# Kernel tuning notes

Measured on AMD Instinct MI355X. Metric: run time of the kernel, lower is better.

The kernel has to match this reference:

```python
import jax, jax.numpy as jnp
import numpy as np

HIDDEN = 2048
NHEADS = 16
NKV = 4
HEAD_DIM = 128
B, T = 2, 2048


def setup_inputs() -> dict:
    key = jax.random.key(0)
    ks = jax.random.split(key, 7)
    x = jax.random.normal(ks[0], (B, T, HIDDEN), dtype=jnp.float32)
    # rope tables [T, head_dim//2]
    inv_freq = 1.0 / (10000.0 ** (jnp.arange(0, HEAD_DIM // 2, dtype=jnp.float32) / (HEAD_DIM // 2)))
    pos = jnp.arange(T, dtype=jnp.float32)
    ang = pos[:, None] * inv_freq[None, :]
    cos, sin = jnp.cos(ang), jnp.sin(ang)
    s = 0.02
    wq = jax.random.normal(ks[1], (HIDDEN, NHEADS * HEAD_DIM), dtype=jnp.float32) * s
    wk = jax.random.normal(ks[2], (HIDDEN, NKV * HEAD_DIM), dtype=jnp.float32) * s
    wv = jax.random.normal(ks[3], (HIDDEN, NKV * HEAD_DIM), dtype=jnp.float32) * s
    wo = jax.random.normal(ks[4], (NHEADS * HEAD_DIM, HIDDEN), dtype=jnp.float32) * s
    return {"x": x, "cos": cos, "sin": sin, "wq": wq, "wk": wk, "wv": wv, "wo": wo}


def _apply_rope(x, cos, sin):
    # x: [B, H, T, D]; cos/sin: [T, D//2]
    hd = x.shape[-1]
    x1, x2 = x[..., : hd // 2], x[..., hd // 2 :]
    c = cos[None, None, : x.shape[2], :]
    s = sin[None, None, : x.shape[2], :]
    return jnp.concatenate([x1 * c - x2 * s, x2 * c + x1 * s], axis=-1)


def reference(x, cos, sin, wq, wk, wv, wo):
    Bb, Tt, _ = x.shape
    q = (x @ wq).reshape(Bb, Tt, NHEADS, HEAD_DIM).transpose(0, 2, 1, 3)  # [B,H,T,D]
    k = (x @ wk).reshape(Bb, Tt, NKV, HEAD_DIM).transpose(0, 2, 1, 3)    # [B,Hk,T,D]
    v = (x @ wv).reshape(Bb, Tt, NKV, HEAD_DIM).transpose(0, 2, 1, 3)
    q = _apply_rope(q, cos, sin)
    k = _apply_rope(k, cos, sin)
    groups = NHEADS // NKV
    k = jnp.repeat(k, groups, axis=1)  # [B,H,T,D]
    v = jnp.repeat(v, groups, axis=1)
    scale = 1.0 / jnp.sqrt(jnp.asarray(HEAD_DIM, dtype=x.dtype))
    scores = jnp.einsum("bhqd,bhkd->bhqk", q, k) * scale
    causal = jnp.tril(jnp.ones((Tt, Tt), dtype=bool))
    scores = jnp.where(causal[None, None, :, :], scores, jnp.asarray(-jnp.inf, dtype=scores.dtype))
    attn = jax.nn.softmax(scores, axis=-1)
    out = jnp.einsum("bhqk,bhkd->bhqd", attn, v)
    out = out.transpose(0, 2, 1, 3).reshape(Bb, Tt, NHEADS * HEAD_DIM)
    return out @ wo
```

## Files before the change

kernel.cpp:

```cpp
#include <hip/hip_runtime.h>

#define HIDDEN 2048
#define NHEADS 16
#define NKV 4
#define HEAD_DIM 128
#define BB 2
#define TT 2048
#define MROWS (BB * TT)
#define NQKV (NHEADS * HEAD_DIM + 2 * NKV * HEAD_DIM)

typedef __attribute__((ext_vector_type(8))) short short8;
typedef __attribute__((ext_vector_type(4))) float f32x4;

#if __has_builtin(__builtin_amdgcn_exp2f)
#define EXP2F __builtin_amdgcn_exp2f
#else
#define EXP2F exp2f
#endif

__device__ __forceinline__ unsigned short f2bf(float f) {
    unsigned int u = __float_as_uint(f);
    unsigned int r = u + 0x7fffu + ((u >> 16) & 1u);
    return (unsigned short)(r >> 16);
}
__device__ __forceinline__ float b2f(unsigned short h) {
    return __uint_as_float(((unsigned int)h) << 16);
}

__device__ __forceinline__ void store_out(float* p, float v) { *p = v; }
__device__ __forceinline__ void store_out(unsigned short* p, float v) { *p = f2bf(v); }

__device__ __forceinline__ void load_lds_16(const void* g, void* l) {
    __builtin_amdgcn_global_load_lds((const __attribute__((address_space(1))) unsigned int*)g,
                                     (__attribute__((address_space(3))) unsigned int*)l,
                                     16, 0, 0);
}

__global__ void cast_x_kernel(const float* __restrict__ x, unsigned short* __restrict__ xb) {
    int i = blockIdx.x * 256 + threadIdx.x;
    float4 v = ((const float4*)x)[i];
    ushort4 o;
    o.x = f2bf(v.x); o.y = f2bf(v.y); o.z = f2bf(v.z); o.w = f2bf(v.w);
    ((ushort4*)xb)[i] = o;
}

__global__ void pack_wqkvT_kernel(const float* __restrict__ wq, const float* __restrict__ wk,
                                  const float* __restrict__ wv, unsigned short* __restrict__ out) {
    __shared__ float tile[32][33];
    int n0 = blockIdx.x * 32, k0 = blockIdx.y * 32;
    int tx = threadIdx.x, ty = threadIdx.y;
#pragma unroll
    for (int i = 0; i < 32; i += 8) {
        int k = k0 + ty + i;
        int n = n0 + tx;
        float v;
        if (n < 2048)      v = wq[(size_t)k * 2048 + n];
        else if (n < 2560) v = wk[(size_t)k * 512 + (n - 2048)];
        else               v = wv[(size_t)k * 512 + (n - 2560)];
        tile[ty + i][tx] = v;
    }
    __syncthreads();
#pragma unroll
    for (int i = 0; i < 32; i += 8) {
        int n = n0 + ty + i;
        int k = k0 + tx;
        out[(size_t)n * HIDDEN + k] = f2bf(tile[tx][ty + i]);
    }
}

__global__ void pack_woT_kernel(const float* __restrict__ wo, unsigned short* __restrict__ out) {
    __shared__ float tile[32][33];
    int n0 = blockIdx.x * 32, k0 = blockIdx.y * 32;
    int tx = threadIdx.x, ty = threadIdx.y;
#pragma unroll
    for (int i = 0; i < 32; i += 8)
        tile[ty + i][tx] = wo[(size_t)(k0 + ty + i) * HIDDEN + n0 + tx];
    __syncthreads();
#pragma unroll
    for (int i = 0; i < 32; i += 8)
        out[(size_t)(n0 + ty + i) * HIDDEN + k0 + tx] = f2bf(tile[tx][ty + i]);
}

template <typename OutT>
__global__ __launch_bounds__(512, 2) void gemm256_kernel(const unsigned short* __restrict__ A,
                                                         const unsigned short* __restrict__ Bt,
                                                         OutT* __restrict__ C,
                                                         int M, int N, int K, int NBX) {
    __shared__ __align__(16) unsigned short sbuf[2][2][256 * 64];
    const int tid = threadIdx.x;
    const int lane = tid & 63, w = tid >> 6;
    const int quad = lane >> 4, l15 = lane & 15;
    const int wrM = w >> 2, wcN = w & 3;

    const int nwg = gridDim.x;
    const int bswz = (blockIdx.x & 7) * (nwg >> 3) + (blockIdx.x >> 3);
    const int m0 = (bswz / NBX) * 256;
    const int n0 = (bswz % NBX) * 256;

    const int lr = tid >> 3;
    const int sc = (tid & 7) ^ (lr & 7);
    const unsigned short* gA = A + (size_t)(m0 + lr) * K + sc * 8;
    const unsigned short* gB = Bt + (size_t)(n0 + lr) * K + sc * 8;
    const size_t jstep = (size_t)64 * K;

    const int s0 = (quad ^ (l15 & 7)) * 8;
    const int s1 = ((4 | quad) ^ (l15 & 7)) * 8;

    f32x4 acc[8][4];
    const f32x4 z4 = {0.f, 0.f, 0.f, 0.f};
#pragma unroll
    for (int mi = 0; mi < 8; ++mi)
#pragma unroll
        for (int ni = 0; ni < 4; ++ni) acc[mi][ni] = z4;

#pragma unroll
    for (int j = 0; j < 4; ++j) {
        load_lds_16(gA + (size_t)j * jstep, &sbuf[0][0][j * 4096 + w * 512]);
        load_lds_16(gB + (size_t)j * jstep, &sbuf[0][1][j * 4096 + w * 512]);
    }
    __asm__ volatile("s_waitcnt vmcnt(0)" ::: "memory");
    __builtin_amdgcn_s_barrier();

    const int NT = K >> 6;
    for (int kt = 0; kt < NT; ++kt) {
        const int buf = kt & 1;
        const unsigned short* bA = &sbuf[buf][0][0];
        const unsigned short* bB = &sbuf[buf][1][0];

        if (kt + 1 < NT) {
            const size_t kof = (size_t)(kt + 1) * 64;
#pragma unroll
            for (int j = 0; j < 4; ++j) {
                load_lds_16(gA + (size_t)j * jstep + kof, &sbuf[buf ^ 1][0][j * 4096 + w * 512]);
                load_lds_16(gB + (size_t)j * jstep + kof, &sbuf[buf ^ 1][1][j * 4096 + w * 512]);
            }
        }

        short8 bf0[4], bf1[4];
#pragma unroll
        for (int ni = 0; ni < 4; ++ni) {
            const unsigned short* br = bB + (wcN * 64 + ni * 16 + l15) * 64;
            bf0[ni] = *(const short8*)(br + s0);
            bf1[ni] = *(const short8*)(br + s1);
        }

#pragma unroll
        for (int ph = 0; ph < 4; ++ph) {
            short8 af0[2], af1[2];
#pragma unroll
            for (int mm = 0; mm < 2; ++mm) {
                const unsigned short* ar = bA + (wrM * 128 + (ph * 2 + mm) * 16 + l15) * 64;
                af0[mm] = *(const short8*)(ar + s0);
                af1[mm] = *(const short8*)(ar + s1);
            }
            if (ph == 3 && kt + 1 < NT) {
                __asm__ volatile("s_waitcnt vmcnt(0)" ::: "memory");
            }
            __builtin_amdgcn_s_barrier();
            __asm__ volatile("s_waitcnt lgkmcnt(0)" ::: "memory");
            __builtin_amdgcn_s_setprio(1);
#pragma unroll
            for (int mm = 0; mm < 2; ++mm)
#pragma unroll
                for (int ni = 0; ni < 4; ++ni) {
                    acc[ph * 2 + mm][ni] =
                        __builtin_amdgcn_mfma_f32_16x16x32_bf16(af0[mm], bf0[ni], acc[ph * 2 + mm][ni], 0, 0, 0);
                    acc[ph * 2 + mm][ni] =
                        __builtin_amdgcn_mfma_f32_16x16x32_bf16(af1[mm], bf1[ni], acc[ph * 2 + mm][ni], 0, 0, 0);
                }
            __builtin_amdgcn_s_setprio(0);
            __builtin_amdgcn_s_barrier();
        }
    }

#pragma unroll
    for (int mi = 0; mi < 8; ++mi)
#pragma unroll
        for (int ni = 0; ni < 4; ++ni)
#pragma unroll
            for (int r = 0; r < 4; ++r) {
                int gr = m0 + wrM * 128 + mi * 16 + quad * 4 + r;
                int gc = n0 + wcN * 64 + ni * 16 + l15;
                store_out(&C[(size_t)gr * N + gc], acc[mi][ni][r]);
            }
}

__global__ __launch_bounds__(512, 2) void gemm256n128_kernel(const unsigned short* __restrict__ A,
                                                             const unsigned short* __restrict__ Bt,
                                                             float* __restrict__ C,
                                                             int M, int N, int K, int NBX) {
    __shared__ __align__(16) unsigned short sA[2][256 * 64];
    __shared__ __align__(16) unsigned short sB[2][128 * 64];
    const int tid = threadIdx.x;
    const int lane = tid & 63, w = tid >> 6;
    const int quad = lane >> 4, l15 = lane & 15;
    const int wrM = w >> 1, wcN = w & 1;

    const int nwg = gridDim.x;
    const int bswz = (blockIdx.x & 7) * (nwg >> 3) + (blockIdx.x >> 3);
    const int m0 = (bswz / NBX) * 256;
    const int n0 = (bswz % NBX) * 128;

    const int lr = tid >> 3;
    const int sc = (tid & 7) ^ (lr & 7);
    const unsigned short* gA = A + (size_t)(m0 + lr) * K + sc * 8;
    const unsigned short* gB = Bt + (size_t)(n0 + lr) * K + sc * 8;
    const size_t jstep = (size_t)64 * K;

    const int s0 = (quad ^ (l15 & 7)) * 8;
    const int s1 = ((4 | quad) ^ (l15 & 7)) * 8;

    f32x4 acc[4][4];
    const f32x4 z4 = {0.f, 0.f, 0.f, 0.f};
#pragma unroll
    for (int mi = 0; mi < 4; ++mi)
#pragma unroll
        for (int ni = 0; ni < 4; ++ni) acc[mi][ni] = z4;

#pragma unroll
    for (int j = 0; j < 4; ++j)
        load_lds_16(gA + (size_t)j * jstep, &sA[0][j * 4096 + w * 512]);
#pragma unroll
    for (int j = 0; j < 2; ++j)
        load_lds_16(gB + (size_t)j * jstep, &sB[0][j * 4096 + w * 512]);
    __asm__ volatile("s_waitcnt vmcnt(0)" ::: "memory");
    __builtin_amdgcn_s_barrier();

    const int NT = K >> 6;
    for (int kt = 0; kt < NT; ++kt) {
        const int buf = kt & 1;
        const unsigned short* bA = &sA[buf][0];
        const unsigned short* bB = &sB[buf][0];

        if (kt + 1 < NT) {
            const size_t kof = (size_t)(kt + 1) * 64;
#pragma unroll
            for (int j = 0; j < 4; ++j)
                load_lds_16(gA + (size_t)j * jstep + kof, &sA[buf ^ 1][j * 4096 + w * 512]);
#pragma unroll
            for (int j = 0; j < 2; ++j)
                load_lds_16(gB + (size_t)j * jstep + kof, &sB[buf ^ 1][j * 4096 + w * 512]);
        }

        short8 bf0[4], bf1[4];
#pragma unroll
        for (int ni = 0; ni < 4; ++ni) {
            const unsigned short* br = bB + (wcN * 64 + ni * 16 + l15) * 64;
            bf0[ni] = *(const short8*)(br + s0);
            bf1[ni] = *(const short8*)(br + s1);
        }

#pragma unroll
        for (int ph = 0; ph < 4; ++ph) {
            short8 af0, af1;
            {
                const unsigned short* ar = bA + (wrM * 64 + ph * 16 + l15) * 64;
                af0 = *(const short8*)(ar + s0);
                af1 = *(const short8*)(ar + s1);
            }
            if (ph == 3 && kt + 1 < NT) {
                __asm__ volatile("s_waitcnt vmcnt(0)" ::: "memory");
            }
            __builtin_amdgcn_s_barrier();
            __asm__ volatile("s_waitcnt lgkmcnt(0)" ::: "memory");
            __builtin_amdgcn_s_setprio(1);
#pragma unroll
            for (int ni = 0; ni < 4; ++ni) {
                acc[ph][ni] = __builtin_amdgcn_mfma_f32_16x16x32_bf16(af0, bf0[ni], acc[ph][ni], 0, 0, 0);
                acc[ph][ni] = __builtin_amdgcn_mfma_f32_16x16x32_bf16(af1, bf1[ni], acc[ph][ni], 0, 0, 0);
            }
            __builtin_amdgcn_s_setprio(0);
            __builtin_amdgcn_s_barrier();
        }
    }

#pragma unroll
    for (int mi = 0; mi < 4; ++mi)
#pragma unroll
        for (int ni = 0; ni < 4; ++ni)
#pragma unroll
            for (int r = 0; r < 4; ++r) {
                int gr = m0 + wrM * 64 + mi * 16 + quad * 4 + r;
                int gc = n0 + wcN * 64 + ni * 16 + l15;
                C[(size_t)gr * N + gc] = acc[mi][ni][r];
            }
}

#define QP (MROWS * NHEADS * 64)
#define KP (MROWS * NKV * 64)
#define QSCL (0.08838834764831845f * 1.4426950408889634f)
__global__ void rope_kernel(const unsigned short* __restrict__ qkv,
                            const float* __restrict__ cosb, const float* __restrict__ sinb,
                            unsigned short* __restrict__ Q, unsigned short* __restrict__ K) {
    int tid = blockIdx.x * 256 + threadIdx.x;
    if (tid < QP) {
        int d = tid & 63;
        int h = (tid >> 6) & 15;
        int row = tid >> 10;
        int t = row & (TT - 1), b = row >> 11;
        float x1 = b2f(qkv[(size_t)row * NQKV + h * 128 + d]);
        float x2 = b2f(qkv[(size_t)row * NQKV + h * 128 + d + 64]);
        float c = cosb[t * 64 + d], s = sinb[t * 64 + d];
        unsigned short* dst = Q + ((size_t)(b * NHEADS + h) * TT + t) * 128 + d;
        dst[0]  = f2bf((x1 * c - x2 * s) * QSCL);
        dst[64] = f2bf((x2 * c + x1 * s) * QSCL);
    } else {
        int p = tid - QP;
        int d = p & 63;
        int kh = (p >> 6) & 3;
        int row = p >> 8;
        int t = row & (TT - 1), b = row >> 11;
        float x1 = b2f(qkv[(size_t)row * NQKV + 2048 + kh * 128 + d]);
        float x2 = b2f(qkv[(size_t)row * NQKV + 2048 + kh * 128 + d + 64]);
        float c = cosb[t * 64 + d], s = sinb[t * 64 + d];
        unsigned short* dst = K + ((size_t)(b * NKV + kh) * TT + t) * 128 + d;
        dst[0]  = f2bf(x1 * c - x2 * s);
        dst[64] = f2bf(x2 * c + x1 * s);
    }
}

__global__ void vtrans_kernel(const unsigned short* __restrict__ qkv,
                              unsigned short* __restrict__ Vt) {
    __shared__ unsigned short tile[32][33];
    int t0 = blockIdx.x * 32, d0 = blockIdx.y * 32, bz = blockIdx.z;
    int b = bz >> 2, kh = bz & 3;
    int tx = threadIdx.x, ty = threadIdx.y;
#pragma unroll
    for (int i = 0; i < 32; i += 8)
        tile[ty + i][tx] = qkv[(size_t)(b * TT + t0 + ty + i) * NQKV + 2560 + kh * 128 + d0 + tx];
    __syncthreads();
#pragma unroll
    for (int i = 0; i < 32; i += 8)
        Vt[((size_t)bz * 128 + d0 + ty + i) * TT + t0 + tx] = tile[tx][ty + i];
}

__global__ __launch_bounds__(256, 3) void flash_kernel(const unsigned short* __restrict__ Qb,
                                                       const unsigned short* __restrict__ Kb,
                                                       const unsigned short* __restrict__ Vtb,
                                                       unsigned short* __restrict__ Ob,
                                                       unsigned short* __restrict__ Po,
                                                       float* __restrict__ Pl) {
    __shared__ __align__(16) unsigned short sK[2][64 * 128];
    __shared__ __align__(16) unsigned short sV[128 * 64];

    const int tid = threadIdx.x;
    const int w = tid >> 6, lane = tid & 63;
    const int quad = lane >> 4, l15 = lane & 15;
    const int r7 = l15 & 7;

    const int lin = blockIdx.x;
    const int member = lin >> 8;
    const int rem = lin & 255;
    const int h = rem & 15;
    const int b = (rem >> 4) & 1;
    const int j = rem >> 5;
    int qb, kvlo, kvhi;
    bool partial;
    if (member == 2) {
        qb = j; kvlo = 0; kvhi = (qb + 1) * 128; partial = false;
    } else {
        qb = 15 - j;
        int half = (qb + 1) * 64;
        kvlo = member ? half : 0;
        kvhi = member ? (qb + 1) * 128 : half;
        partial = true;
    }
    const int q0 = qb * 128;
    const int ntile = (kvhi - kvlo) >> 6;
    const int kvh = h >> 2;
    const unsigned short* Qh = Qb + (size_t)(b * NHEADS + h) * TT * 128;
    const unsigned short* Kh = Kb + (size_t)(b * NKV + kvh) * TT * 128;
    const unsigned short* Vth = Vtb + (size_t)(b * NKV + kvh) * 128 * TT;

    const int wrow0 = q0 + w * 32;

    const int kr = lane >> 4;
    const unsigned short* gKe = Kh + (size_t)(w * 16 + kr) * 128 + (((lane & 15) ^ kr) * 8);
    const unsigned short* gKo = Kh + (size_t)(w * 16 + 4 + kr) * 128 + (((lane & 15) ^ (4 + kr)) * 8);
    const int vr = lane >> 3;
    const unsigned short* gV0 = Vth + (size_t)(w * 32 + vr) * TT + (((lane & 7) ^ vr) * 8);

    short8 aq[2][4];
#pragma unroll
    for (int mi = 0; mi < 2; ++mi)
#pragma unroll
        for (int dk = 0; dk < 4; ++dk)
            aq[mi][dk] = *(const short8*)(Qh + (size_t)(wrow0 + mi * 16 + l15) * 128 + dk * 32 + quad * 8);

    f32x4 accO[2][8];
    float accLc[2] = {0.f, 0.f};
    const f32x4 z4 = {0.f, 0.f, 0.f, 0.f};
#pragma unroll
    for (int mi = 0; mi < 2; ++mi)
#pragma unroll
        for (int nb = 0; nb < 8; ++nb) accO[mi][nb] = z4;

#pragma unroll
    for (int g = 0; g < 4; ++g) {
        const unsigned short* src = (g & 1) ? gKo : gKe;
        load_lds_16(src + (size_t)(kvlo + (g >> 1) * 8) * 128, &sK[0][(w * 4 + g) * 512]);
    }

    for (int it = 0; it < ntile; ++it) {
        const int cur = it & 1;
        const int kv0 = kvlo + it * 64;
        __asm__ volatile("s_waitcnt vmcnt(0)" ::: "memory");
        __builtin_amdgcn_s_barrier();
#pragma unroll
        for (int g = 0; g < 4; ++g)
            load_lds_16(gV0 + (size_t)(g * 8) * TT + kv0, &sV[(w * 4 + g) * 512]);
        const bool hasn = (it + 1 < ntile);
        if (hasn) {
#pragma unroll
            for (int g = 0; g < 4; ++g) {
                const unsigned short* src = (g & 1) ? gKo : gKe;
                load_lds_16(src + (size_t)(kv0 + 64 + (g >> 1) * 8) * 128, &sK[cur ^ 1][(w * 4 + g) * 512]);
            }
        }
        const bool compute = (kv0 <= wrow0 + 31);
        short8 ap[2][2];
        if (compute) {
            f32x4 st[4][2];
#pragma unroll
            for (int t = 0; t < 4; ++t)
#pragma unroll
                for (int h2 = 0; h2 < 2; ++h2) st[t][h2] = z4;
            __builtin_amdgcn_s_setprio(1);
#pragma unroll
            for (int t = 0; t < 4; ++t) {
#pragma unroll
                for (int dk = 0; dk < 4; ++dk) {
                    short8 ak = *(const short8*)(&sK[cur][(t * 16 + l15) * 128 + ((dk * 4 + quad) ^ r7) * 8]);
                    st[t][0] = __builtin_amdgcn_mfma_f32_16x16x32_bf16(ak, aq[0][dk], st[t][0], 0, 0, 0);
                    st[t][1] = __builtin_amdgcn_mfma_f32_16x16x32_bf16(ak, aq[1][dk], st[t][1], 0, 0, 0);
                }
            }
            __builtin_amdgcn_s_setprio(0);
            unsigned int pk32[4][2][2];
#pragma unroll
            for (int h2 = 0; h2 < 2; ++h2) {
                const int qg = wrow0 + h2 * 16 + l15;
#pragma unroll
                for (int t = 0; t < 4; ++t) {
                    const int kvb = kv0 + t * 16 + quad * 4;
                    const bool nm = (kv0 + t * 16 + 15) > (wrow0 + h2 * 16);
                    float pv[4];
#pragma unroll
                    for (int r = 0; r < 4; ++r) {
                        float p = EXP2F(st[t][h2][r]);
                        if (nm) p = (kvb + r <= qg) ? p : 0.f;
                        pv[r] = p;
                    }
                    accLc[h2] += (pv[0] + pv[1]) + (pv[2] + pv[3]);
                    __asm__("v_cvt_pk_bf16_f32 %0, %1, %2" : "=v"(pk32[t][h2][0]) : "v"(pv[0]), "v"(pv[1]));
                    __asm__("v_cvt_pk_bf16_f32 %0, %1, %2" : "=v"(pk32[t][h2][1]) : "v"(pv[2]), "v"(pv[3]));
                }
            }
#pragma unroll
            for (int h2 = 0; h2 < 2; ++h2)
#pragma unroll
                for (int kf = 0; kf < 2; ++kf) {
                    union { unsigned int u[4]; short8 s8; } W;
#pragma unroll
                    for (int wdx = 0; wdx < 4; ++wdx) {
                        int srcl = (2 * (quad & 1) + (wdx >> 1)) * 16 + l15;
                        unsigned int a0 = (unsigned int)__shfl((int)pk32[2 * kf][h2][wdx & 1], srcl, 64);
                        unsigned int a1 = (unsigned int)__shfl((int)pk32[2 * kf + 1][h2][wdx & 1], srcl, 64);
                        W.u[wdx] = (quad >> 1) ? a1 : a0;
                    }
                    ap[h2][kf] = W.s8;
                }
        }
        if (hasn) { __asm__ volatile("s_waitcnt vmcnt(4)" ::: "memory"); }
        else      { __asm__ volatile("s_waitcnt vmcnt(0)" ::: "memory"); }
        __builtin_amdgcn_s_barrier();
        if (compute) {
            __builtin_amdgcn_s_setprio(1);
#pragma unroll
            for (int nb = 0; nb < 8; ++nb) {
                short8 bv0 = *(const short8*)(&sV[(nb * 16 + l15) * 64 + ((quad) ^ r7) * 8]);
                short8 bv1 = *(const short8*)(&sV[(nb * 16 + l15) * 64 + ((4 + quad) ^ r7) * 8]);
#pragma unroll
                for (int mi = 0; mi < 2; ++mi) {
                    accO[mi][nb] = __builtin_amdgcn_mfma_f32_16x16x32_bf16(ap[mi][0], bv0, accO[mi][nb], 0, 0, 0);
                    accO[mi][nb] = __builtin_amdgcn_mfma_f32_16x16x32_bf16(ap[mi][1], bv1, accO[mi][nb], 0, 0, 0);
                }
            }
            __builtin_amdgcn_s_setprio(0);
        }
    }

    float Lr[2][4];
#pragma unroll
    for (int mi = 0; mi < 2; ++mi) {
        float v = accLc[mi];
        v += __shfl_xor(v, 16, 64);
        v += __shfl_xor(v, 32, 64);
#pragma unroll
        for (int r = 0; r < 4; ++r)
            Lr[mi][r] = __shfl(v, quad * 4 + r, 64);
    }

    __syncthreads();
    unsigned short* sPw = &sV[w * 2048];

    if (!partial) {
        float inv[2][4];
#pragma unroll
        for (int mi = 0; mi < 2; ++mi)
#pragma unroll
            for (int r = 0; r < 4; ++r) inv[mi][r] = 1.0f / Lr[mi][r];
        const size_t obase = ((size_t)b * TT + wrow0) * (NHEADS * HEAD_DIM) + h * 128;
#pragma unroll
        for (int half = 0; half < 2; ++half) {
            __asm__ volatile("s_waitcnt lgkmcnt(0)" ::: "memory");
#pragma unroll
            for (int mi = 0; mi < 2; ++mi)
#pragma unroll
                for (int nb2 = 0; nb2 < 4; ++nb2)
#pragma unroll
                    for (int r = 0; r < 4; ++r) {
                        const int row = mi * 16 + quad * 4 + r;
                        sPw[row * 64 + (((2 * nb2 + (l15 >> 3)) ^ (row & 7)) * 8) + r7] =
                            f2bf(accO[mi][half * 4 + nb2][r] * inv[mi][r]);
                    }
            __asm__ volatile("s_waitcnt lgkmcnt(0)" ::: "memory");
#pragma unroll
            for (int pass = 0; pass < 4; ++pass) {
                int row2 = pass * 8 + (lane >> 3);
                short8 vv = *(const short8*)(&sPw[row2 * 64 + (((lane & 7) ^ (row2 & 7)) * 8)]);
                *(short8*)(Ob + obase + (size_t)row2 * (NHEADS * HEAD_DIM) + half * 64 + (lane & 7) * 8) = vv;
            }
        }
    } else {
        const size_t pbase = ((size_t)(member * 2 + b) * 1024 + (wrow0 - 1024)) * 2048 + h * 128;
#pragma unroll
        for (int half = 0; half < 2; ++half) {
            __asm__ volatile("s_waitcnt lgkmcnt(0)" ::: "memory");
#pragma unroll
            for (int mi = 0; mi < 2; ++mi)
#pragma unroll
                for (int nb2 = 0; nb2 < 4; ++nb2)
#pragma unroll
                    for (int r = 0; r < 4; ++r) {
                        const int row = mi * 16 + quad * 4 + r;
                        sPw[row * 64 + (((2 * nb2 + (l15 >> 3)) ^ (row & 7)) * 8) + r7] =
                            f2bf(accO[mi][half * 4 + nb2][r]);
                    }
            __asm__ volatile("s_waitcnt lgkmcnt(0)" ::: "memory");
#pragma unroll
            for (int pass = 0; pass < 4; ++pass) {
                int row2 = pass * 8 + (lane >> 3);
                short8 vv = *(const short8*)(&sPw[row2 * 64 + (((lane & 7) ^ (row2 & 7)) * 8)]);
                *(short8*)(Po + pbase + (size_t)row2 * 2048 + half * 64 + (lane & 7) * 8) = vv;
            }
        }
        float* plb = Pl + ((size_t)(member * 2 + b) * 16 + h) * 1024 + (wrow0 - 1024);
        if (l15 == 0) {
#pragma unroll
            for (int mi = 0; mi < 2; ++mi)
#pragma unroll
                for (int r = 0; r < 4; ++r)
                    plb[mi * 16 + quad * 4 + r] = Lr[mi][r];
        }
    }
}

__global__ void merge_kernel(const unsigned short* __restrict__ Po, const float* __restrict__ Pl,
                             unsigned short* __restrict__ attn) {
    int gid = blockIdx.x * 256 + threadIdx.x;
    size_t e8 = (size_t)gid * 8;
    int col = (int)(e8 & 2047);
    int rl  = (int)((e8 >> 11) & 1023);
    int b   = (int)(e8 >> 21);
    int h   = col >> 7;
    size_t i0 = ((size_t)b * 1024 + rl) * 2048 + col;
    size_t i1 = ((size_t)(2 + b) * 1024 + rl) * 2048 + col;
    float l = Pl[((size_t)b * 16 + h) * 1024 + rl] + Pl[((size_t)(2 + b) * 16 + h) * 1024 + rl];
    float inv = 1.0f / l;
    union { uint4 v; unsigned short u[8]; } a, c, o;
    a.v = *(const uint4*)(Po + i0);
    c.v = *(const uint4*)(Po + i1);
#pragma unroll
    for (int k = 0; k < 8; ++k)
        o.u[k] = f2bf((b2f(a.u[k]) + b2f(c.u[k])) * inv);
    *(uint4*)(attn + ((size_t)b * 2048 + 1024 + rl) * 2048 + col) = o.v;
}

extern "C" void kernel_launch(void* const* d_in, const int* in_sizes, int n_in,
                              void* d_out, int out_size, void* d_ws, size_t ws_size,
                              hipStream_t stream) {
    const float* x    = (const float*)d_in[0];
    const float* cosb = (const float*)d_in[1];
    const float* sinb = (const float*)d_in[2];
    const float* wq   = (const float*)d_in[3];
    const float* wk   = (const float*)d_in[4];
    const float* wv   = (const float*)d_in[5];
    const float* wo   = (const float*)d_in[6];
    float* out = (float*)d_out;

    char* ws = (char*)d_ws;
    unsigned short* xb    = (unsigned short*)(ws);
    unsigned short* wqkvT = (unsigned short*)(ws + (16u << 20));
    unsigned short* woT   = (unsigned short*)(ws + (28u << 20));
    unsigned short* qkv   = (unsigned short*)(ws + (36u << 20));
    unsigned short* Qbuf  = (unsigned short*)(ws + (60u << 20));
    unsigned short* Kbuf  = (unsigned short*)(ws + (76u << 20));
    unsigned short* Vt    = (unsigned short*)(ws + (80u << 20));
    unsigned short* attn  = (unsigned short*)(ws + (84u << 20));
    unsigned short* Po    = (unsigned short*)(ws);
    float*          Pl    = (float*)(ws + (16u << 20));

    cast_x_kernel<<<(MROWS * HIDDEN) / 4 / 256, 256, 0, stream>>>(x, xb);
    pack_wqkvT_kernel<<<dim3(NQKV / 32, HIDDEN / 32), dim3(32, 8), 0, stream>>>(wq, wk, wv, wqkvT);
    pack_woT_kernel<<<dim3(HIDDEN / 32, HIDDEN / 32), dim3(32, 8), 0, stream>>>(wo, woT);

    gemm256_kernel<unsigned short><<<dim3((MROWS / 256) * (NQKV / 256)), 512, 0, stream>>>(
        xb, wqkvT, qkv, MROWS, NQKV, HIDDEN, NQKV / 256);

    rope_kernel<<<(QP + KP) / 256, 256, 0, stream>>>(qkv, cosb, sinb, Qbuf, Kbuf);
    vtrans_kernel<<<dim3(TT / 32, HEAD_DIM / 32, BB * NKV), dim3(32, 8), 0, stream>>>(qkv, Vt);

    flash_kernel<<<dim3(768), 256, 0, stream>>>(Qbuf, Kbuf, Vt, attn, Po, Pl);
    merge_kernel<<<dim3(2048), 256, 0, stream>>>(Po, Pl, attn);

    gemm256n128_kernel<<<dim3((MROWS / 256) * (HIDDEN / 128)), 512, 0, stream>>>(
        attn, woT, out, MROWS, HIDDEN, HIDDEN, HIDDEN / 128);
}
```

Before: 318.8 us.

## Retile QKV GEMM to 256x192 tiles and move prefetch wait to loop top

```diff
diff --git a/kernel.cpp b/kernel.cpp
--- a/kernel.cpp
+++ b/kernel.cpp
@@ -81,12 +81,12 @@
         out[(size_t)(n0 + ty + i) * HIDDEN + k0 + tx] = f2bf(tile[tx][ty + i]);
 }
 
-template <typename OutT>
-__global__ __launch_bounds__(512, 2) void gemm256_kernel(const unsigned short* __restrict__ A,
+__global__ __launch_bounds__(512, 1) void gemm192_kernel(const unsigned short* __restrict__ A,
                                                          const unsigned short* __restrict__ Bt,
-                                                         OutT* __restrict__ C,
-                                                         int M, int N, int K, int NBX) {
-    __shared__ __align__(16) unsigned short sbuf[2][2][256 * 64];
+                                                         unsigned short* __restrict__ C) {
+    const int M = MROWS, N = NQKV, K = HIDDEN, NBX = 16;
+    __shared__ __align__(16) unsigned short sA[2][256 * 64];
+    __shared__ __align__(16) unsigned short sB[2][192 * 64];
     const int tid = threadIdx.x;
     const int lane = tid & 63, w = tid >> 6;
     const int quad = lane >> 4, l15 = lane & 15;
@@ -95,7 +95,7 @@
     const int nwg = gridDim.x;
     const int bswz = (blockIdx.x & 7) * (nwg >> 3) + (blockIdx.x >> 3);
     const int m0 = (bswz / NBX) * 256;
-    const int n0 = (bswz % NBX) * 256;
+    const int n0 = (bswz % NBX) * 192;
 
     const int lr = tid >> 3;
     const int sc = (tid & 7) ^ (lr & 7);
@@ -106,40 +106,44 @@
     const int s0 = (quad ^ (l15 & 7)) * 8;
     const int s1 = ((4 | quad) ^ (l15 & 7)) * 8;
 
-    f32x4 acc[8][4];
+    f32x4 acc[8][3];
     const f32x4 z4 = {0.f, 0.f, 0.f, 0.f};
 #pragma unroll
     for (int mi = 0; mi < 8; ++mi)
 #pragma unroll
-        for (int ni = 0; ni < 4; ++ni) acc[mi][ni] = z4;
-
-#pragma unroll
-    for (int j = 0; j < 4; ++j) {
-        load_lds_16(gA + (size_t)j * jstep, &sbuf[0][0][j * 4096 + w * 512]);
-        load_lds_16(gB + (size_t)j * jstep, &sbuf[0][1][j * 4096 + w * 512]);
-    }
-    __asm__ volatile("s_waitcnt vmcnt(0)" ::: "memory");
-    __builtin_amdgcn_s_barrier();
+        for (int ni = 0; ni < 3; ++ni) acc[mi][ni] = z4;
+
+#pragma unroll
+    for (int j = 0; j < 4; ++j)
+        load_lds_16(gA + (size_t)j * jstep, &sA[0][j * 4096 + w * 512]);
+#pragma unroll
+    for (int j = 0; j < 3; ++j)
+        load_lds_16(gB + (size_t)j * jstep, &sB[0][j * 4096 + w * 512]);
 
     const int NT = K >> 6;
     for (int kt = 0; kt < NT; ++kt) {
         const int buf = kt & 1;
-        const unsigned short* bA = &sbuf[buf][0][0];
-        const unsigned short* bB = &sbuf[buf][1][0];
+        const unsigned short* bA = &sA[buf][0];
+        const unsigned short* bB = &sB[buf][0];
 
         if (kt + 1 < NT) {
             const size_t kof = (size_t)(kt + 1) * 64;
 #pragma unroll
-            for (int j = 0; j < 4; ++j) {
-                load_lds_16(gA + (size_t)j * jstep + kof, &sbuf[buf ^ 1][0][j * 4096 + w * 512]);
-                load_lds_16(gB + (size_t)j * jstep + kof, &sbuf[buf ^ 1][1][j * 4096 + w * 512]);
-            }
-        }
-
-        short8 bf0[4], bf1[4];
-#pragma unroll
-        for (int ni = 0; ni < 4; ++ni) {
-            const unsigned short* br = bB + (wcN * 64 + ni * 16 + l15) * 64;
+            for (int j = 0; j < 4; ++j)
+                load_lds_16(gA + (size_t)j * jstep + kof, &sA[buf ^ 1][j * 4096 + w * 512]);
+#pragma unroll
+            for (int j = 0; j < 3; ++j)
+                load_lds_16(gB + (size_t)j * jstep + kof, &sB[buf ^ 1][j * 4096 + w * 512]);
+            __asm__ volatile("s_waitcnt vmcnt(7)" ::: "memory");
+        } else {
+            __asm__ volatile("s_waitcnt vmcnt(0)" ::: "memory");
+        }
+        __builtin_amdgcn_s_barrier();
+
+        short8 bf0[3], bf1[3];
+#pragma unroll
+        for (int ni = 0; ni < 3; ++ni) {
+            const unsigned short* br = bB + (wcN * 48 + ni * 16 + l15) * 64;
             bf0[ni] = *(const short8*)(br + s0);
             bf1[ni] = *(const short8*)(br + s1);
         }
@@ -153,16 +157,13 @@
                 af0[mm] = *(const short8*)(ar + s0);
                 af1[mm] = *(const short8*)(ar + s1);
             }
-            if (ph == 3 && kt + 1 < NT) {
-                __asm__ volatile("s_waitcnt vmcnt(0)" ::: "memory");
-            }
             __builtin_amdgcn_s_barrier();
             __asm__ volatile("s_waitcnt lgkmcnt(0)" ::: "memory");
             __builtin_amdgcn_s_setprio(1);
 #pragma unroll
             for (int mm = 0; mm < 2; ++mm)
 #pragma unroll
-                for (int ni = 0; ni < 4; ++ni) {
+                for (int ni = 0; ni < 3; ++ni) {
                     acc[ph * 2 + mm][ni] =
                         __builtin_amdgcn_mfma_f32_16x16x32_bf16(af0[mm], bf0[ni], acc[ph * 2 + mm][ni], 0, 0, 0);
                     acc[ph * 2 + mm][ni] =
@@ -176,16 +177,16 @@
 #pragma unroll
     for (int mi = 0; mi < 8; ++mi)
 #pragma unroll
-        for (int ni = 0; ni < 4; ++ni)
+        for (int ni = 0; ni < 3; ++ni)
 #pragma unroll
             for (int r = 0; r < 4; ++r) {
                 int gr = m0 + wrM * 128 + mi * 16 + quad * 4 + r;
-                int gc = n0 + wcN * 64 + ni * 16 + l15;
-                store_out(&C[(size_t)gr * N + gc], acc[mi][ni][r]);
-            }
-}
-
-__global__ __launch_bounds__(512, 2) void gemm256n128_kernel(const unsigned short* __restrict__ A,
+                int gc = n0 + wcN * 48 + ni * 16 + l15;
+                C[(size_t)gr * N + gc] = f2bf(acc[mi][ni][r]);
+            }
+}
+
+__global__ __launch_bounds__(512, 1) void gemm256n128_kernel(const unsigned short* __restrict__ A,
                                                              const unsigned short* __restrict__ Bt,
                                                              float* __restrict__ C,
                                                              int M, int N, int K, int NBX) {
@@ -223,8 +224,6 @@
 #pragma unroll
     for (int j = 0; j < 2; ++j)
         load_lds_16(gB + (size_t)j * jstep, &sB[0][j * 4096 + w * 512]);
-    __asm__ volatile("s_waitcnt vmcnt(0)" ::: "memory");
-    __builtin_amdgcn_s_barrier();
 
     const int NT = K >> 6;
     for (int kt = 0; kt < NT; ++kt) {
@@ -240,7 +239,11 @@
 #pragma unroll
             for (int j = 0; j < 2; ++j)
                 load_lds_16(gB + (size_t)j * jstep + kof, &sB[buf ^ 1][j * 4096 + w * 512]);
-        }
+            __asm__ volatile("s_waitcnt vmcnt(6)" ::: "memory");
+        } else {
+            __asm__ volatile("s_waitcnt vmcnt(0)" ::: "memory");
+        }
+        __builtin_amdgcn_s_barrier();
 
         short8 bf0[4], bf1[4];
 #pragma unroll
@@ -257,9 +260,6 @@
                 const unsigned short* ar = bA + (wrM * 64 + ph * 16 + l15) * 64;
                 af0 = *(const short8*)(ar + s0);
                 af1 = *(const short8*)(ar + s1);
-            }
-            if (ph == 3 && kt + 1 < NT) {
-                __asm__ volatile("s_waitcnt vmcnt(0)" ::: "memory");
             }
             __builtin_amdgcn_s_barrier();
             __asm__ volatile("s_waitcnt lgkmcnt(0)" ::: "memory");
@@ -502,7 +502,7 @@
     }
 
     __syncthreads();
-    unsigned short* sPw = &sV[w * 2048];
+    unsigned short* sPw = &sV[0] + w * 2048;
 
     if (!partial) {
         float inv[2][4];
@@ -615,8 +615,7 @@
     pack_wqkvT_kernel<<<dim3(NQKV / 32, HIDDEN / 32), dim3(32, 8), 0, stream>>>(wq, wk, wv, wqkvT);
     pack_woT_kernel<<<dim3(HIDDEN / 32, HIDDEN / 32), dim3(32, 8), 0, stream>>>(wo, woT);
 
-    gemm256_kernel<unsigned short><<<dim3((MROWS / 256) * (NQKV / 256)), 512, 0, stream>>>(
-        xb, wqkvT, qkv, MROWS, NQKV, HIDDEN, NQKV / 256);
+    gemm192_kernel<<<dim3(256), 512, 0, stream>>>(xb, wqkvT, qkv);
 
     rope_kernel<<<(QP + KP) / 256, 256, 0, stream>>>(qkv, cosb, sinb, Qbuf, Kbuf);
     vtrans_kernel<<<dim3(TT / 32, HEAD_DIM / 32, BB * NKV), dim3(32, 8), 0, stream>>>(qkv, Vt);
```

After: 323.3 us. Within noise of the previous version (+1.4%).
